# Kernel tuning notes

Measured on AMD Instinct MI355X. Metric: run time of the kernel, lower is better.

## Reference

```python
import jax, jax.numpy as jnp
import numpy as np

A, NA, D_OBS, B = 16, 8, 64, 128  # agents, actions, obs dim, graphs
DZ = D_OBS + NA  # obs_z_input_dim = 72


def _mlp(x, W1, b1, W2, b2):
    # Linear -> leaky_relu(0.01) -> Linear, torch Linear convention (y = x @ W.T + b)
    return jax.nn.leaky_relu(x @ W1.T + b1) @ W2.T + b2


def setup_inputs() -> dict:
    key = jax.random.key(0)
    ks = iter(jax.random.split(key, 40))
    p = {}
    p["obs"] = jax.random.normal(next(ks), (B * A, D_OBS), jnp.float32)
    p["policies"] = jax.random.uniform(next(ks), (B * A, NA), jnp.float32)
    p["actions"] = jax.random.uniform(next(ks), (B * A, NA), jnp.float32)

    def mk(name, inp, out):
        p[name + "_w"] = jax.random.normal(next(ks), (out, inp), jnp.float32) / np.sqrt(inp).astype(np.float32)
        p[name + "_b"] = jax.random.normal(next(ks), (out,), jnp.float32) * 0.01

    mk("kw1", D_OBS, 64); mk("kw2", 64, 64)   # key_weight layers
    mk("qw1", D_OBS, 64); mk("qw2", 64, 64)   # query_weight layers
    mk("ko1", DZ, 64);    mk("ko2", 64, 64)   # key_obsz layers
    mk("qo1", DZ, 64);    mk("qo2", 64, 64)   # query_obsz layers
    mk("av1", DZ, 64);    mk("av2", 64, 64)   # attention_value_obsz layers
    mk("fv1", 128, 64);   mk("fv2", 64, 8)    # final_value layers
    return p


def reference(obs, policies, actions,
              kw1_w, kw1_b, kw2_w, kw2_b, qw1_w, qw1_b, qw2_w, qw2_b,
              ko1_w, ko1_b, ko2_w, ko2_b, qo1_w, qo1_b, qo2_w, qo2_b,
              av1_w, av1_b, av2_w, av2_b, fv1_w, fv1_b, fv2_w, fv2_b):
    d_k_w = jnp.sqrt(jnp.float32(kw2_w.shape[0]))
    d_k_o = jnp.sqrt(jnp.float32(ko2_w.shape[0]))
    Bn = obs.shape[0] // A
    obs_b = obs.reshape(Bn, A, -1)                      # [B,A,Dobs]
    pi = policies.reshape(Bn, A, NA)
    act = actions.reshape(Bn, A, NA)

    # --- DGL update_all on the fully-connected (with self-loop) per-batch graph ---
    key_z = _mlp(obs_b, kw1_w, kw1_b, kw2_w, kw2_b)     # [B,A,dk]
    query_z = _mlp(obs_b, qw1_w, qw1_b, qw2_w, qw2_b)
    score = jnp.einsum('bjd,bid->bij', key_z, query_z)  # src key j -> dst query i
    w = jax.nn.sigmoid(score / d_k_w)[..., None]        # [B,A,A,1], mailbox gate
    z = w * act[:, None] + (1.0 - w) * pi[:, None]      # [B,A(i),A(j),NA]
    weight_z = w.reshape(Bn * A, A, 1)

    # obs_z[b,i,j] = cat(obs[b,j], z[b,i,j])
    obs_rep = jnp.broadcast_to(obs_b[:, None], (Bn, A, A, obs_b.shape[-1]))
    obs_z = jnp.concatenate([obs_rep, z], axis=-1)      # [B,A,A,DZ]

    diag = jnp.arange(A)
    src = obs_z[:, diag, diag]                          # source_obs_z_: [B,A,DZ] (j==i entry)

    key_o = _mlp(src, ko1_w, ko1_b, ko2_w, ko2_b)       # broadcast over j
    query_o = _mlp(obs_z, qo1_w, qo1_b, qo2_w, qo2_b)   # [B,A,A,dk]
    score_o = jnp.einsum('bid,bijd->bij', key_o, query_o)
    weights_o = jax.nn.softmax(jnp.exp(jnp.clip(score_o / d_k_o, -5.0, 5.0)), axis=-1)  # [B,A,A]

    # obs_z_pi[b,i,j,k] = op[b,j] if k==j else obs_z[b,i,k], op = cat(obs, pi)
    op = jnp.concatenate([obs_b, pi], axis=-1)          # [B,A,DZ]
    m = jnp.eye(A, dtype=obs.dtype)[None, None, :, :, None]          # (j,k) mask
    obs_z_pi = obs_z[:, :, None] * (1.0 - m) + op[:, None, None] * m  # [B,A,A,A,DZ]

    attn_src = _mlp(src, av1_w, av1_b, av2_w, av2_b)                  # [B,A,O]
    attn_other = _mlp(obs_z_pi, av1_w, av1_b, av2_w, av2_b)           # [B,A,A,A,O]

    w_exp = weights_o[:, None, :, :, None]              # [b,i,j,k,1] = weights_o[b,j,k]
    mixed = jnp.mean(attn_other * w_exp, axis=-2)       # mean over k -> [B,A,A,O]
    src_rep = jnp.broadcast_to(attn_src[:, None], mixed.shape)
    node_features = jnp.concatenate([src_rep, mixed], axis=-1)        # [B,A,A,2O]
    value = _mlp(node_features, fv1_w, fv1_b, fv2_w, fv2_b)           # [B,A,A,8]

    weights_obsz = jnp.broadcast_to(w_exp, (Bn, A, A, A, 1))
    return value, weight_z, weights_obsz
```

## Files before the change

kernel.cpp:

```cpp
#include <hip/hip_runtime.h>

#define A_ 16
#define NA_ 8
#define DOBS_ 64

typedef _Float16 f16;
typedef f16 h2 __attribute__((ext_vector_type(2)));
typedef f16 v8h __attribute__((ext_vector_type(8)));
typedef float v4f __attribute__((ext_vector_type(4)));

__device__ __forceinline__ float fdot2f(h2 a, h2 b, float c) {
  return __builtin_amdgcn_fdot2(a, b, c, false);
}
__device__ __forceinline__ float lrelu(float x) { return x > 0.f ? x : 0.01f * x; }

struct P {
  const float *obs, *pol, *act;
  const float *kw1w, *kw1b, *kw2w, *kw2b, *qw1w, *qw1b, *qw2w, *qw2b;
  const float *ko1w, *ko1b, *ko2w, *ko2b, *qo1w, *qo1b, *qo2w, *qo2b;
  const float *av1w, *av1b, *av2w, *av2b, *fv1w, *fv1b, *fv2w, *fv2b;
  float *out0, *out1, *out2;
};

#define OBSH 0
#define OBSL 1152
#define X1Ho 2304
#define X1Lo 3456
#define X2Ho 4608
#define X2Lo 5760
#define EHO  6912
#define FLT  7168
#define F_PI   0
#define F_ACT  128
#define F_WSIG 256
#define F_WO   512
#define F_C0   768
#define F_S2   784
#define F_S3G  1872
#define F_WZK  2960
#define F_WZQ  3472
#define WKW1  15136
#define WQW1  19744
#define WKW2  24352
#define WQW2  28960
#define WKO1H 33568
#define WKO1L 38176
#define WKO2H 42784
#define WKO2L 47392
#define WQO1H 52000
#define WQO1L 56608
#define WQO2H 61216
#define WQO2L 65824
#define LDS_F16 70432
#define AV1H  15136
#define AV2H  21280
#define FV1H  25888
#define FV2PW 34592
#define BACKB 35104
#define SLICE 52000
#define AOSRC 64288
#define APTO  65440
#define AEXT  66976

__device__ __forceinline__ v4f gemm_plain(const f16* Xh, const f16* W, float bv, int nt, int lane) {
  const int m = lane & 15, q = lane >> 4;
  v4f acc = {bv, bv, bv, bv};
  const v8h a0 = *(const v8h*)(Xh + m * 72 + q * 8);
  const v8h a1 = *(const v8h*)(Xh + m * 72 + 32 + q * 8);
  const f16* wr = W + (nt * 16 + m) * 72 + q * 8;
  acc = __builtin_amdgcn_mfma_f32_16x16x32_f16(a0, *(const v8h*)wr, acc, 0, 0, 0);
  acc = __builtin_amdgcn_mfma_f32_16x16x32_f16(a1, *(const v8h*)(wr + 32), acc, 0, 0, 0);
  return acc;
}

__device__ __forceinline__ v4f gemm_tile(const f16* Xh, const f16* Xl,
                                         const f16* Wh, const f16* Wl,
                                         float bv, int nt, int lane) {
  const int m = lane & 15, q = lane >> 4;
  v4f acc = {bv, bv, bv, bv};
  const v8h ah0 = *(const v8h*)(Xh + m * 72 + q * 8);
  const v8h ah1 = *(const v8h*)(Xh + m * 72 + 32 + q * 8);
  const v8h al0 = *(const v8h*)(Xl + m * 72 + q * 8);
  const v8h al1 = *(const v8h*)(Xl + m * 72 + 32 + q * 8);
  const f16* wr = Wh + (nt * 16 + m) * 72 + q * 8;
  const v8h bh0 = *(const v8h*)(wr);
  const v8h bh1 = *(const v8h*)(wr + 32);
  const f16* wr2 = Wl + (nt * 16 + m) * 72 + q * 8;
  const v8h bl0 = *(const v8h*)(wr2);
  const v8h bl1 = *(const v8h*)(wr2 + 32);
  acc = __builtin_amdgcn_mfma_f32_16x16x32_f16(ah0, bh0, acc, 0, 0, 0);
  acc = __builtin_amdgcn_mfma_f32_16x16x32_f16(ah1, bh1, acc, 0, 0, 0);
  acc = __builtin_amdgcn_mfma_f32_16x16x32_f16(ah0, bl0, acc, 0, 0, 0);
  acc = __builtin_amdgcn_mfma_f32_16x16x32_f16(ah1, bl1, acc, 0, 0, 0);
  acc = __builtin_amdgcn_mfma_f32_16x16x32_f16(al0, bh0, acc, 0, 0, 0);
  acc = __builtin_amdgcn_mfma_f32_16x16x32_f16(al1, bh1, acc, 0, 0, 0);
  return acc;
}

__device__ __forceinline__ void writeX(f16* Xh, f16* Xl, v4f acc, int nt, int lane, bool relu) {
  const int m = lane & 15, q = lane >> 4;
#pragma unroll
  for (int reg = 0; reg < 4; reg++) {
    float y = acc[reg];
    if (relu) y = lrelu(y);
    const f16 yh = (f16)y;
    Xh[(q * 4 + reg) * 72 + nt * 16 + m] = yh;
    Xl[(q * 4 + reg) * 72 + nt * 16 + m] = (f16)(y - (float)yh);
  }
}

__device__ __forceinline__ void putP(f16* W, float4 v, int o, int rq) {
  h2* d = (h2*)(W + o * 72 + 4 * rq);
  d[0] = h2{(f16)v.x, (f16)v.y};
  d[1] = h2{(f16)v.z, (f16)v.w};
}

__device__ __forceinline__ void putW(f16* Wh, f16* Wl, float4 v, int o, int rq) {
  h2* dh = (h2*)(Wh + o * 72 + 4 * rq);
  h2* dl = (h2*)(Wl + o * 72 + 4 * rq);
  const f16 hx = (f16)v.x, hy = (f16)v.y, hz = (f16)v.z, hw = (f16)v.w;
  dh[0] = h2{hx, hy};
  dh[1] = h2{hz, hw};
  dl[0] = h2{(f16)(v.x - (float)hx), (f16)(v.y - (float)hy)};
  dl[1] = h2{(f16)(v.z - (float)hz), (f16)(v.w - (float)hw)};
}

__device__ __forceinline__ v8h bfrag(const f16* Wm, int stride, int nt, int ks, int lane) {
  const int n = lane & 15, q = lane >> 4;
  return *(const v8h*)(Wm + (nt * 16 + n) * stride + ks * 32 + q * 8);
}

__device__ __forceinline__ void av_mlp2(const f16* obsh, const f16* av1H, const f16* av2H,
                                        const float* av1b, const float* av2b,
                                        f16* Hbuf, v8h az, int lane, v4f acc2[4]) {
  const int m = lane & 15, q = lane >> 4;
  const v8h a0 = *(const v8h*)(obsh + m * 72 + q * 8);
  const v8h a1 = *(const v8h*)(obsh + m * 72 + 32 + q * 8);
#pragma unroll
  for (int nt = 0; nt < 4; nt++) {
    const float bv = av1b[nt * 16 + m];
    v4f acc = {bv, bv, bv, bv};
    acc = __builtin_amdgcn_mfma_f32_16x16x32_f16(a0, bfrag(av1H, 96, nt, 0, lane), acc, 0, 0, 0);
    acc = __builtin_amdgcn_mfma_f32_16x16x32_f16(a1, bfrag(av1H, 96, nt, 1, lane), acc, 0, 0, 0);
    acc = __builtin_amdgcn_mfma_f32_16x16x32_f16(az, bfrag(av1H, 96, nt, 2, lane), acc, 0, 0, 0);
#pragma unroll
    for (int reg = 0; reg < 4; reg++)
      Hbuf[(q * 4 + reg) * 72 + nt * 16 + m] = (f16)lrelu(acc[reg]);
  }
  const v8h h0 = *(const v8h*)(Hbuf + m * 72 + q * 8);
  const v8h h1 = *(const v8h*)(Hbuf + m * 72 + 32 + q * 8);
#pragma unroll
  for (int nt = 0; nt < 4; nt++) {
    const float bv = av2b[nt * 16 + m];
    v4f acc = {bv, bv, bv, bv};
    acc = __builtin_amdgcn_mfma_f32_16x16x32_f16(h0, bfrag(av2H, 72, nt, 0, lane), acc, 0, 0, 0);
    acc = __builtin_amdgcn_mfma_f32_16x16x32_f16(h1, bfrag(av2H, 72, nt, 1, lane), acc, 0, 0, 0);
    acc2[nt] = acc;
  }
}

__global__ __launch_bounds__(512) void critic_fused(P p) {
  extern __shared__ f16 SMB[];
  float* F = (float*)(SMB + FLT);
  const int tid = threadIdx.x;
  const int b = blockIdx.x >> 1, ihalf = blockIdx.x & 1;
  const int w = tid >> 6, lane = tid & 63;
  const int m = lane & 15, quad = lane >> 4;
  const int o = tid & 63, r8 = tid >> 6;

  const float2 Robs = ((const float2*)(p.obs + (size_t)b * 1024))[tid];
  float Rpa = 0.f;
  if (tid < 128) Rpa = p.pol[(size_t)b * 128 + tid];
  else if (tid < 256) Rpa = p.act[(size_t)b * 128 + tid - 128];
  const float Rwzko = p.ko1w[(tid >> 3) * 72 + 64 + (tid & 7)];
  const float Rwzqo = p.qo1w[(tid >> 3) * 72 + 64 + (tid & 7)];
  float4 Rkw1[2], Rqw1[2], Rkw2[2], Rqw2[2], Rko1[2], Rko2[2], Rqo1[2], Rqo2[2];
#pragma unroll
  for (int h = 0; h < 2; h++) {
    const int rq = r8 + 8 * h;
    Rkw1[h] = *(const float4*)(p.kw1w + o * 64 + 4 * rq);
    Rqw1[h] = *(const float4*)(p.qw1w + o * 64 + 4 * rq);
    Rkw2[h] = *(const float4*)(p.kw2w + o * 64 + 4 * rq);
    Rqw2[h] = *(const float4*)(p.qw2w + o * 64 + 4 * rq);
    Rko1[h] = *(const float4*)(p.ko1w + o * 72 + 4 * rq);
    Rko2[h] = *(const float4*)(p.ko2w + o * 64 + 4 * rq);
    Rqo1[h] = *(const float4*)(p.qo1w + o * 72 + 4 * rq);
    Rqo2[h].x = p.qo2w[(4 * rq + 0) * 64 + o];
    Rqo2[h].y = p.qo2w[(4 * rq + 1) * 64 + o];
    Rqo2[h].z = p.qo2w[(4 * rq + 2) * 64 + o];
    Rqo2[h].w = p.qo2w[(4 * rq + 3) * 64 + o];
  }
  const int bi = (w & 3) * 16 + m;
  const float bias1 = (w < 4 ? p.kw1b : p.qw1b)[bi];
  const float bias2 = (w < 4 ? p.kw2b : p.qw2b)[bi];
  const float bias3 = (w < 4 ? p.ko1b : p.qo1b)[bi];
  const float bias4 = p.ko2b[bi];
  const float Bqo2_0 = p.qo2b[tid & 31];
  const float Bqo2_1 = p.qo2b[(tid & 31) + 32];

  {
    const int e0 = 2 * tid, r0 = e0 >> 6, c0i = e0 & 63;
    const f16 hx = (f16)Robs.x, hy = (f16)Robs.y;
    *(h2*)(SMB + OBSH + r0 * 72 + c0i) = h2{hx, hy};
    *(h2*)(SMB + OBSL + r0 * 72 + c0i) = h2{(f16)(Robs.x - (float)hx), (f16)(Robs.y - (float)hy)};
  }
  if (tid < 128) F[F_PI + tid] = Rpa;
  else if (tid < 256) F[F_ACT + tid - 128] = Rpa;
  F[F_WZK + tid] = Rwzko;
  { const int oo = tid >> 3, c = tid & 7; F[F_WZQ + (oo & 15) * 32 + (oo >> 4) * 8 + c] = Rwzqo; }
#pragma unroll
  for (int h = 0; h < 2; h++) {
    const int rq = r8 + 8 * h;
    putP(SMB + WKW1, Rkw1[h], o, rq);
    putP(SMB + WQW1, Rqw1[h], o, rq);
    putP(SMB + WKW2, Rkw2[h], o, rq);
    putP(SMB + WQW2, Rqw2[h], o, rq);
    putW(SMB + WKO1H, SMB + WKO1L, Rko1[h], o, rq);
    putW(SMB + WKO2H, SMB + WKO2L, Rko2[h], o, rq);
    putW(SMB + WQO1H, SMB + WQO1L, Rqo1[h], o, rq);
    putW(SMB + WQO2H, SMB + WQO2L, Rqo2[h], o, rq);
  }
  __syncthreads();

  {
    const f16* Wp = (w < 4) ? (SMB + WKW1) : (SMB + WQW1);
    f16* Xo = (w < 4) ? (SMB + X1Ho) : (SMB + X2Ho);
    v4f a = gemm_plain(SMB + OBSH, Wp, bias1, w & 3, lane);
#pragma unroll
    for (int reg = 0; reg < 4; reg++)
      Xo[(quad * 4 + reg) * 72 + (w & 3) * 16 + m] = (f16)lrelu(a[reg]);
  }
  __syncthreads();

  {
    const f16* Wp = (w < 4) ? (SMB + WKW2) : (SMB + WQW2);
    const f16* Xi = (w < 4) ? (SMB + X1Ho) : (SMB + X2Ho);
    float* So = (w < 4) ? (F + F_S2) : (F + F_S3G);
    v4f a = gemm_plain(Xi, Wp, bias2, w & 3, lane);
#pragma unroll
    for (int reg = 0; reg < 4; reg++)
      So[(quad * 4 + reg) * 68 + (w & 3) * 16 + m] = a[reg];
  }
  __syncthreads();

  {
    const int idx = tid >> 1, g2 = tid & 1;
    const int i = idx >> 4, j = idx & 15;
    float a0 = 0.f, a1 = 0.f, a2 = 0.f, a3 = 0.f;
#pragma unroll
    for (int t4 = 0; t4 < 8; t4++) {
      const float4 qv = *(const float4*)(F + F_S3G + i * 68 + g2 * 32 + 4 * t4);
      const float4 kv = *(const float4*)(F + F_S2 + j * 68 + g2 * 32 + 4 * t4);
      a0 += qv.x * kv.x; a1 += qv.y * kv.y; a2 += qv.z * kv.z; a3 += qv.w * kv.w;
    }
    float sc = (a0 + a1) + (a2 + a3);
    sc += __shfl_xor(sc, 1);
    if (g2 == 0) {
      const float wv = 1.f / (1.f + __expf(-sc * 0.125f));
      F[F_WSIG + idx] = wv;
      p.out1[(size_t)b * 256 + idx] = wv;
    }
  }
  __syncthreads();

  if (w < 4) {
    v4f a = gemm_tile(SMB + OBSH, SMB + OBSL, SMB + WKO1H, SMB + WKO1L, bias3, w, lane);
    const int oo = w * 16 + m;
    float wzv[8];
    *(float4*)wzv = *(const float4*)(F + F_WZK + oo * 8);
    *(float4*)(wzv + 4) = *(const float4*)(F + F_WZK + oo * 8 + 4);
#pragma unroll
    for (int reg = 0; reg < 4; reg++) {
      const int rr = quad * 4 + reg;
      const float wrr = F[F_WSIG + rr * 16 + rr];
      float zp = 0.f;
#pragma unroll
      for (int c = 0; c < 8; c++) {
        const float zc = F[F_PI + rr * 8 + c] + wrr * (F[F_ACT + rr * 8 + c] - F[F_PI + rr * 8 + c]);
        zp += wzv[c] * zc;
      }
      const float y = lrelu(a[reg] + zp);
      const f16 yh = (f16)y;
      SMB[X2Ho + rr * 72 + oo] = yh;
      SMB[X2Lo + rr * 72 + oo] = (f16)(y - (float)yh);
    }
  } else {
    v4f a = gemm_tile(SMB + OBSH, SMB + OBSL, SMB + WQO1H, SMB + WQO1L, bias3, w - 4, lane);
#pragma unroll
    for (int reg = 0; reg < 4; reg++)
      F[F_S3G + m * 68 + (quad * 4 + reg) * 4 + (w - 4)] = a[reg];
  }
  __syncthreads();

  const float4 rav1a = ((const float4*)p.av1w)[tid * 2];
  const float4 rav1b = ((const float4*)p.av1w)[tid * 2 + 1];
  const float rav1c = p.av1w[4096 + tid];
  const float4 rav2a = ((const float4*)p.av2w)[tid * 2];
  const float4 rav2b = ((const float4*)p.av2w)[tid * 2 + 1];
  const float rfv2 = p.fv2w[tid];
  float rb1 = 0.f, rb2 = 0.f, rb3 = 0.f, rb4 = 0.f;
  if (tid < 64) { rb1 = p.av1b[tid]; rb2 = p.av2b[tid]; rb3 = p.fv1b[tid]; }
  if (tid < 8) rb4 = p.fv2b[tid];
  if (w < 4) {
    v4f a = gemm_tile(SMB + X2Ho, SMB + X2Lo, SMB + WKO2H, SMB + WKO2L, bias4, w, lane);
    writeX(SMB + X1Ho, SMB + X1Lo, a, w, lane, false);
  }
  __syncthreads();

  float4 rfv[4];
#pragma unroll
  for (int qq = 0; qq < 4; qq++) rfv[qq] = ((const float4*)p.fv1w)[tid * 4 + qq];
  if (w < 4) {
    v4f a = gemm_tile(SMB + X1Ho, SMB + X1Lo, SMB + WQO2H, SMB + WQO2L, 0.f, w, lane);
#pragma unroll
    for (int reg = 0; reg < 4; reg++)
      F[F_S2 + (quad * 4 + reg) * 68 + w * 16 + m] = a[reg];
  }
  {
    const int rr = tid >> 5, cc = tid & 31;
    const float kv0 = (float)SMB[X1Ho + rr * 72 + cc] + (float)SMB[X1Lo + rr * 72 + cc];
    const float kv1 = (float)SMB[X1Ho + rr * 72 + cc + 32] + (float)SMB[X1Lo + rr * 72 + cc + 32];
    float t = kv0 * Bqo2_0 + kv1 * Bqo2_1;
#pragma unroll
    for (int mk = 1; mk < 32; mk <<= 1) t += __shfl_xor(t, mk);
    if (cc == 0) F[F_C0 + rr] = t;
  }
  __syncthreads();

  {
    const int idx = tid >> 1, g2 = tid & 1;
    const int i = idx >> 4, j = idx & 15;
    const float wij = F[F_WSIG + i * 16 + j];
    float z[8];
#pragma unroll
    for (int c = 0; c < 8; c++)
      z[c] = F[F_PI + j * 8 + c] + wij * (F[F_ACT + j * 8 + c] - F[F_PI + j * 8 + c]);
    float sc = 0.f;
#pragma unroll
    for (int gg = 2 * g2; gg <= 2 * g2 + 1; gg++) {
#pragma unroll
      for (int t = 0; t < 16; t++) {
        const float4 wa = *(const float4*)(F + F_WZQ + t * 32 + gg * 8);
        const float4 wb = *(const float4*)(F + F_WZQ + t * 32 + gg * 8 + 4);
        float hv = F[F_S3G + t * 68 + j * 4 + gg]
          + wa.x * z[0] + wa.y * z[1] + wa.z * z[2] + wa.w * z[3]
          + wb.x * z[4] + wb.y * z[5] + wb.z * z[6] + wb.w * z[7];
        hv = lrelu(hv);
        sc += F[F_S2 + i * 68 + gg * 16 + t] * hv;
      }
    }
    sc += __shfl_xor(sc, 1);
    if (g2 == 0) {
      float yv = (sc + F[F_C0 + i]) * 0.125f;
      yv = fminf(fmaxf(yv, -5.f), 5.f);
      SMB[EHO + idx] = (f16)__expf(yv);
    }
  }
  __syncthreads();

  if (tid < 256) {
    const int i = tid >> 4, j = tid & 15;
    float ev[16]; float mx = -1e30f;
#pragma unroll
    for (int jj = 0; jj < 16; jj++) { ev[jj] = (float)SMB[EHO + i * 16 + jj]; mx = fmaxf(mx, ev[jj]); }
    float den = 0.f;
#pragma unroll
    for (int jj = 0; jj < 16; jj++) den += __expf(ev[jj] - mx);
    F[F_WO + tid] = __expf(ev[j] - mx) / den;
  }
  {
    float av1v[8] = {rav1a.x, rav1a.y, rav1a.z, rav1a.w, rav1b.x, rav1b.y, rav1b.z, rav1b.w};
#pragma unroll
    for (int e = 0; e < 8; e++) {
      const int k = tid * 8 + e, rr = k / 72, cc = k - rr * 72;
      SMB[AV1H + rr * 96 + cc] = (f16)av1v[e];
    }
    const int k = 4096 + tid, rr = k / 72, cc = k - rr * 72;
    SMB[AV1H + rr * 96 + cc] = (f16)rav1c;
    const int row = tid >> 3, c0p = 72 + (tid & 7) * 3;
#pragma unroll
    for (int c = 0; c < 3; c++) SMB[AV1H + row * 96 + c0p + c] = (f16)0.f;
    float av2v[8] = {rav2a.x, rav2a.y, rav2a.z, rav2a.w, rav2b.x, rav2b.y, rav2b.z, rav2b.w};
#pragma unroll
    for (int e = 0; e < 8; e++) {
      const int k2 = tid * 8 + e;
      SMB[AV2H + (k2 >> 6) * 72 + (k2 & 63)] = (f16)av2v[e];
    }
    SMB[FV2PW + tid] = (f16)rfv2;
    float* BF = (float*)(SMB + BACKB);
    if (tid < 64) { BF[tid] = rb1; BF[64 + tid] = rb2; BF[128 + tid] = rb3; }
    if (tid < 8) BF[192 + tid] = rb4;
  }
  __syncthreads();

  {
    const int kk = tid >> 5, j2 = tid & 31;
    float v = 0.f;
    if (j2 < 16) v = F[F_WO + kk * 16 + j2] * 0.0625f;
    else if (j2 - 16 == kk) v = F[F_WO + kk * 16 + kk] * 0.0625f;
    SMB[AEXT + kk * 40 + j2] = (f16)v;
    const int q_ = tid >> 1, g2_ = tid & 1, k_ = q_ & 15;
    float* dst = p.out2 + ((size_t)b * 256 + q_) * 16 + 8 * g2_;
    *(float4*)(dst) = *(const float4*)(F + F_WO + k_ * 16 + 8 * g2_);
    *(float4*)(dst + 4) = *(const float4*)(F + F_WO + k_ * 16 + 8 * g2_ + 4);
  }
  __syncthreads();

#pragma unroll
  for (int qq = 0; qq < 4; qq++) {
    const int e0 = tid * 16 + qq * 4;
    h2* d = (h2*)&SMB[FV1H + (e0 >> 7) * 136 + (e0 & 127)];
    d[0] = h2{(f16)rfv[qq].x, (f16)rfv[qq].y};
    d[1] = h2{(f16)rfv[qq].z, (f16)rfv[qq].w};
  }
  const float* BF = (const float*)(SMB + BACKB);
  const int i_ = ihalf * 8 + w;
  f16* Sl = SMB + SLICE + w * 1536;
  {
    v8h az = {};
    if (quad == 0) {
      const float wv = F[F_WSIG + i_ * 16 + m];
#pragma unroll
      for (int c = 0; c < 8; c++)
        az[c] = (f16)(F[F_PI + m * 8 + c] + wv * (F[F_ACT + m * 8 + c] - F[F_PI + m * 8 + c]));
    }
    v4f acc2[4];
    av_mlp2(SMB + OBSH, SMB + AV1H, SMB + AV2H, BF, BF + 64, Sl, az, lane, acc2);
#pragma unroll
    for (int nt = 0; nt < 4; nt++)
#pragma unroll
      for (int reg = 0; reg < 4; reg++)
        Sl[(nt * 16 + m) * 24 + quad * 4 + reg] = (f16)acc2[nt][reg];
  }
  if (w == 0) {
    v8h az = {};
    if (quad == 0) {
#pragma unroll
      for (int c = 0; c < 8; c++) az[c] = (f16)F[F_PI + m * 8 + c];
    }
    v4f acc2[4];
    av_mlp2(SMB + OBSH, SMB + AV1H, SMB + AV2H, BF, BF + 64, SMB + APTO, az, lane, acc2);
#pragma unroll
    for (int nt = 0; nt < 4; nt++)
#pragma unroll
      for (int reg = 0; reg < 4; reg++)
        SMB[APTO + (nt * 16 + m) * 24 + quad * 4 + reg] = (f16)acc2[nt][reg];
  }
  if (w == 1) {
    v8h az = {};
    if (quad == 0) {
      const float wv = F[F_WSIG + m * 16 + m];
#pragma unroll
      for (int c = 0; c < 8; c++)
        az[c] = (f16)(F[F_PI + m * 8 + c] + wv * (F[F_ACT + m * 8 + c] - F[F_PI + m * 8 + c]));
    }
    v4f acc2[4];
    av_mlp2(SMB + OBSH, SMB + AV1H, SMB + AV2H, BF, BF + 64, SMB + AOSRC, az, lane, acc2);
#pragma unroll
    for (int nt = 0; nt < 4; nt++)
#pragma unroll
      for (int reg = 0; reg < 4; reg++)
        SMB[AOSRC + (quad * 4 + reg) * 72 + nt * 16 + m] = (f16)acc2[nt][reg];
  }
  __syncthreads();

  {
    const v8h am = *(const v8h*)(&SMB[AEXT + m * 40 + quad * 8]);
    v4f macc[4];
#pragma unroll
    for (int nt = 0; nt < 4; nt++) {
      const int oo = nt * 16 + m;
      v8h bf;
      if (quad < 2) {
        bf = *(const v8h*)(Sl + oo * 24 + quad * 8);
      } else {
        const v8h apv = *(const v8h*)(&SMB[APTO + oo * 24 + (quad - 2) * 8]);
        const v8h aov = *(const v8h*)(Sl + oo * 24 + (quad - 2) * 8);
        bf = apv - aov;
      }
      v4f z4 = {0.f, 0.f, 0.f, 0.f};
      macc[nt] = __builtin_amdgcn_mfma_f32_16x16x32_f16(am, bf, z4, 0, 0, 0);
    }
#pragma unroll
    for (int nt = 0; nt < 4; nt++)
#pragma unroll
      for (int reg = 0; reg < 4; reg++)
        Sl[(quad * 4 + reg) * 72 + nt * 16 + m] = (f16)macc[nt][reg];
  }
  {
    const v8h f0 = *(const v8h*)(&SMB[AOSRC + m * 72 + quad * 8]);
    const v8h f1 = *(const v8h*)(&SMB[AOSRC + m * 72 + 32 + quad * 8]);
    const v8h f2 = *(const v8h*)(Sl + m * 72 + quad * 8);
    const v8h f3 = *(const v8h*)(Sl + m * 72 + 32 + quad * 8);
#pragma unroll
    for (int nt = 0; nt < 4; nt++) {
      const float bv = BF[128 + nt * 16 + m];
      v4f acc = {bv, bv, bv, bv};
      acc = __builtin_amdgcn_mfma_f32_16x16x32_f16(f0, bfrag(SMB + FV1H, 136, nt, 0, lane), acc, 0, 0, 0);
      acc = __builtin_amdgcn_mfma_f32_16x16x32_f16(f1, bfrag(SMB + FV1H, 136, nt, 1, lane), acc, 0, 0, 0);
      acc = __builtin_amdgcn_mfma_f32_16x16x32_f16(f2, bfrag(SMB + FV1H, 136, nt, 2, lane), acc, 0, 0, 0);
      acc = __builtin_amdgcn_mfma_f32_16x16x32_f16(f3, bfrag(SMB + FV1H, 136, nt, 3, lane), acc, 0, 0, 0);
#pragma unroll
      for (int reg = 0; reg < 4; reg++)
        Sl[(quad * 4 + reg) * 72 + nt * 16 + m] = (f16)lrelu(acc[reg]);
    }
  }
  {
    const int g2 = quad;
    float y0 = BF[192 + 2 * g2], y1 = BF[192 + 2 * g2 + 1];
#pragma unroll
    for (int o2 = 0; o2 < 32; o2++) {
      const h2 hh = *(const h2*)(Sl + m * 72 + 2 * o2);
      const h2 w0 = *(const h2*)(&SMB[FV2PW + (2 * g2) * 64 + 2 * o2]);
      const h2 w1 = *(const h2*)(&SMB[FV2PW + (2 * g2 + 1) * 64 + 2 * o2]);
      y0 = fdot2f(w0, hh, y0);
      y1 = fdot2f(w1, hh, y1);
    }
    *(float2*)(p.out0 + ((size_t)b * 256 + i_ * 16 + m) * 8 + 2 * g2) = make_float2(y0, y1);
  }
}

extern "C" void kernel_launch(void* const* d_in, const int* in_sizes, int n_in,
                              void* d_out, int out_size, void* d_ws, size_t ws_size,
                              hipStream_t stream) {
  P p;
  p.obs = (const float*)d_in[0];
  p.pol = (const float*)d_in[1];
  p.act = (const float*)d_in[2];
  p.kw1w = (const float*)d_in[3];  p.kw1b = (const float*)d_in[4];
  p.kw2w = (const float*)d_in[5];  p.kw2b = (const float*)d_in[6];
  p.qw1w = (const float*)d_in[7];  p.qw1b = (const float*)d_in[8];
  p.qw2w = (const float*)d_in[9];  p.qw2b = (const float*)d_in[10];
  p.ko1w = (const float*)d_in[11]; p.ko1b = (const float*)d_in[12];
  p.ko2w = (const float*)d_in[13]; p.ko2b = (const float*)d_in[14];
  p.qo1w = (const float*)d_in[15]; p.qo1b = (const float*)d_in[16];
  p.qo2w = (const float*)d_in[17]; p.qo2b = (const float*)d_in[18];
  p.av1w = (const float*)d_in[19]; p.av1b = (const float*)d_in[20];
  p.av2w = (const float*)d_in[21]; p.av2b = (const float*)d_in[22];
  p.fv1w = (const float*)d_in[23]; p.fv1b = (const float*)d_in[24];
  p.fv2w = (const float*)d_in[25]; p.fv2b = (const float*)d_in[26];

  const int Bn = in_sizes[0] / (A_ * DOBS_);
  p.out0 = (float*)d_out;
  p.out1 = p.out0 + (size_t)Bn * A_ * A_ * NA_;
  p.out2 = p.out1 + (size_t)Bn * A_ * A_;

  const size_t lds_bytes = (size_t)LDS_F16 * sizeof(f16);
  (void)hipFuncSetAttribute(reinterpret_cast<const void*>(critic_fused),
                            hipFuncAttributeMaxDynamicSharedMemorySize, (int)lds_bytes);
  hipLaunchKernelGGL(critic_fused, dim3(2 * Bn), dim3(512), lds_bytes, stream, p);
}
```

Before: 125.3 us.

## Overlap attention-value MLP with key/query chain via warp specialization

Reorganizes the post-sigmoid phase so warp 0 runs the whole ko1→ko2→qo2 chain, warp 1 runs qo1, and the remaining six warps run the attention-value MLP tasks concurrently, instead of spreading each stage over eight warps with barriers in between. All weight and bias loads are hoisted to the start of the kernel, and the av weights are staged into LDS earlier, with a new LDS layout holding separate slice buffers. Several __syncthreads are removed and the out2 store is folded into the final per-warp stage. The serial dependency chain on warp 0 and the larger LDS footprint (reducing occupancy) may offset the gain from overlap.

```diff
diff --git a/kernel.cpp b/kernel.cpp
--- a/kernel.cpp
+++ b/kernel.cpp
@@ -39,28 +39,30 @@
 #define F_S3G  1872
 #define F_WZK  2960
 #define F_WZQ  3472
-#define WKW1  15136
-#define WQW1  19744
-#define WKW2  24352
-#define WQW2  28960
-#define WKO1H 33568
-#define WKO1L 38176
-#define WKO2H 42784
-#define WKO2L 47392
-#define WQO1H 52000
-#define WQO1L 56608
-#define WQO2H 61216
-#define WQO2L 65824
-#define LDS_F16 70432
-#define AV1H  15136
-#define AV2H  21280
-#define FV1H  25888
-#define FV2PW 34592
-#define BACKB 35104
-#define SLICE 52000
-#define AOSRC 64288
-#define APTO  65440
-#define AEXT  66976
+#define F_B    3984
+#define WKW1  15648
+#define WQW1  20256
+#define WKW2  24864
+#define WQW2  29472
+#define WKO1H 34080
+#define WKO1L 38688
+#define WKO2H 43296
+#define WKO2L 47904
+#define WQO1H 52512
+#define WQO1L 57120
+#define WQO2H 61728
+#define WQO2L 66336
+#define AV1H  15648
+#define AV2H  21792
+#define BACKB1 26400
+#define SLA   26656
+#define SLB   70944
+#define AOSRC 77088
+#define APTO  78240
+#define FV1H  34080
+#define FV2PW 42784
+#define BACKB2 43296
+#define LDS_F16 79776
 
 __device__ __forceinline__ v4f gemm_plain(const f16* Xh, const f16* W, float bv, int nt, int lane) {
   const int m = lane & 15, q = lane >> 4;
@@ -193,10 +195,20 @@
   const int bi = (w & 3) * 16 + m;
   const float bias1 = (w < 4 ? p.kw1b : p.qw1b)[bi];
   const float bias2 = (w < 4 ? p.kw2b : p.qw2b)[bi];
-  const float bias3 = (w < 4 ? p.ko1b : p.qo1b)[bi];
-  const float bias4 = p.ko2b[bi];
-  const float Bqo2_0 = p.qo2b[tid & 31];
-  const float Bqo2_1 = p.qo2b[(tid & 31) + 32];
+  float rbo1 = 0.f, rbo2 = 0.f, rbo3 = 0.f, rbo4 = 0.f;
+  if (tid < 64) { rbo1 = p.ko1b[tid]; rbo2 = p.ko2b[tid]; rbo3 = p.qo1b[tid]; rbo4 = p.qo2b[tid]; }
+  const float4 rav1a = ((const float4*)p.av1w)[tid * 2];
+  const float4 rav1b = ((const float4*)p.av1w)[tid * 2 + 1];
+  const float rav1c = p.av1w[4096 + tid];
+  const float4 rav2a = ((const float4*)p.av2w)[tid * 2];
+  const float4 rav2b = ((const float4*)p.av2w)[tid * 2 + 1];
+  float4 rfv[4];
+#pragma unroll
+  for (int qq = 0; qq < 4; qq++) rfv[qq] = ((const float4*)p.fv1w)[tid * 4 + qq];
+  const float rfv2 = p.fv2w[tid];
+  float rb1 = 0.f, rb2 = 0.f, rb3 = 0.f, rb4 = 0.f;
+  if (tid < 64) { rb1 = p.av1b[tid]; rb2 = p.av2b[tid]; rb3 = p.fv1b[tid]; }
+  if (tid < 8) rb4 = p.fv2b[tid];
 
   {
     const int e0 = 2 * tid, r0 = e0 >> 6, c0i = e0 & 63;
@@ -208,6 +220,10 @@
   else if (tid < 256) F[F_ACT + tid - 128] = Rpa;
   F[F_WZK + tid] = Rwzko;
   { const int oo = tid >> 3, c = tid & 7; F[F_WZQ + (oo & 15) * 32 + (oo >> 4) * 8 + c] = Rwzqo; }
+  if (tid < 64) {
+    F[F_B + tid] = rbo1; F[F_B + 64 + tid] = rbo2;
+    F[F_B + 128 + tid] = rbo3; F[F_B + 192 + tid] = rbo4;
+  }
 #pragma unroll
   for (int h = 0; h < 2; h++) {
     const int rq = r8 + 8 * h;
@@ -261,69 +277,131 @@
       p.out1[(size_t)b * 256 + idx] = wv;
     }
   }
-  __syncthreads();
-
-  if (w < 4) {
-    v4f a = gemm_tile(SMB + OBSH, SMB + OBSL, SMB + WKO1H, SMB + WKO1L, bias3, w, lane);
-    const int oo = w * 16 + m;
-    float wzv[8];
-    *(float4*)wzv = *(const float4*)(F + F_WZK + oo * 8);
-    *(float4*)(wzv + 4) = *(const float4*)(F + F_WZK + oo * 8 + 4);
-#pragma unroll
-    for (int reg = 0; reg < 4; reg++) {
-      const int rr = quad * 4 + reg;
-      const float wrr = F[F_WSIG + rr * 16 + rr];
-      float zp = 0.f;
-#pragma unroll
-      for (int c = 0; c < 8; c++) {
-        const float zc = F[F_PI + rr * 8 + c] + wrr * (F[F_ACT + rr * 8 + c] - F[F_PI + rr * 8 + c]);
-        zp += wzv[c] * zc;
-      }
-      const float y = lrelu(a[reg] + zp);
-      const f16 yh = (f16)y;
-      SMB[X2Ho + rr * 72 + oo] = yh;
-      SMB[X2Lo + rr * 72 + oo] = (f16)(y - (float)yh);
+  {
+    float av1v[8] = {rav1a.x, rav1a.y, rav1a.z, rav1a.w, rav1b.x, rav1b.y, rav1b.z, rav1b.w};
+#pragma unroll
+    for (int e = 0; e < 8; e++) {
+      const int k = tid * 8 + e, rr = k / 72, cc = k - rr * 72;
+      SMB[AV1H + rr * 96 + cc] = (f16)av1v[e];
+    }
+    const int k = 4096 + tid, rr = k / 72, cc = k - rr * 72;
+    SMB[AV1H + rr * 96 + cc] = (f16)rav1c;
+    const int row = tid >> 3, c0p = 72 + (tid & 7) * 3;
+#pragma unroll
+    for (int c = 0; c < 3; c++) SMB[AV1H + row * 96 + c0p + c] = (f16)0.f;
+    float av2v[8] = {rav2a.x, rav2a.y, rav2a.z, rav2a.w, rav2b.x, rav2b.y, rav2b.z, rav2b.w};
+#pragma unroll
+    for (int e = 0; e < 8; e++) {
+      const int k2 = tid * 8 + e;
+      SMB[AV2H + (k2 >> 6) * 72 + (k2 & 63)] = (f16)av2v[e];
+    }
+    float* BF1 = (float*)(SMB + BACKB1);
+    if (tid < 64) { BF1[tid] = rb1; BF1[64 + tid] = rb2; }
+  }
+  __syncthreads();
+
+  const float* BF1 = (const float*)(SMB + BACKB1);
+  if (w == 0) {
+#pragma unroll
+    for (int nt = 0; nt < 4; nt++) {
+      v4f a = gemm_tile(SMB + OBSH, SMB + OBSL, SMB + WKO1H, SMB + WKO1L, F[F_B + nt * 16 + m], nt, lane);
+      const int oo = nt * 16 + m;
+      float wzv[8];
+      *(float4*)wzv = *(const float4*)(F + F_WZK + oo * 8);
+      *(float4*)(wzv + 4) = *(const float4*)(F + F_WZK + oo * 8 + 4);
+#pragma unroll
+      for (int reg = 0; reg < 4; reg++) {
+        const int rr = quad * 4 + reg;
+        const float wrr = F[F_WSIG + rr * 17];
+        float zp = 0.f;
+#pragma unroll
+        for (int c = 0; c < 8; c++) {
+          const float zc = F[F_PI + rr * 8 + c] + wrr * (F[F_ACT + rr * 8 + c] - F[F_PI + rr * 8 + c]);
+          zp += wzv[c] * zc;
+        }
+        const float y = lrelu(a[reg] + zp);
+        const f16 yh = (f16)y;
+        SMB[X2Ho + rr * 72 + oo] = yh;
+        SMB[X2Lo + rr * 72 + oo] = (f16)(y - (float)yh);
+      }
+    }
+#pragma unroll
+    for (int nt = 0; nt < 4; nt++) {
+      v4f a = gemm_tile(SMB + X2Ho, SMB + X2Lo, SMB + WKO2H, SMB + WKO2L, F[F_B + 64 + nt * 16 + m], nt, lane);
+      writeX(SMB + X1Ho, SMB + X1Lo, a, nt, lane, false);
+    }
+#pragma unroll
+    for (int nt = 0; nt < 4; nt++) {
+      v4f a = gemm_tile(SMB + X1Ho, SMB + X1Lo, SMB + WQO2H, SMB + WQO2L, 0.f, nt, lane);
+#pragma unroll
+      for (int reg = 0; reg < 4; reg++)
+        F[F_S2 + (quad * 4 + reg) * 68 + nt * 16 + m] = a[reg];
+    }
+    {
+      const int r = lane >> 2, cs = (lane & 3) * 16;
+      float t = 0.f;
+#pragma unroll
+      for (int c = 0; c < 16; c++) {
+        const float kv = (float)SMB[X1Ho + r * 72 + cs + c] + (float)SMB[X1Lo + r * 72 + cs + c];
+        t += kv * F[F_B + 192 + cs + c];
+      }
+      t += __shfl_xor(t, 1);
+      t += __shfl_xor(t, 2);
+      if ((lane & 3) == 0) F[F_C0 + r] = t;
+    }
+  } else if (w == 1) {
+#pragma unroll
+    for (int nt = 0; nt < 4; nt++) {
+      v4f a = gemm_tile(SMB + OBSH, SMB + OBSL, SMB + WQO1H, SMB + WQO1L, F[F_B + 128 + nt * 16 + m], nt, lane);
+#pragma unroll
+      for (int reg = 0; reg < 4; reg++)
+        F[F_S3G + m * 68 + (quad * 4 + reg) * 4 + nt] = a[reg];
     }
   } else {
-    v4f a = gemm_tile(SMB + OBSH, SMB + OBSL, SMB + WQO1H, SMB + WQO1L, bias3, w - 4, lane);
-#pragma unroll
-    for (int reg = 0; reg < 4; reg++)
-      F[F_S3G + m * 68 + (quad * 4 + reg) * 4 + (w - 4)] = a[reg];
-  }
-  __syncthreads();
-
-  const float4 rav1a = ((const float4*)p.av1w)[tid * 2];
-  const float4 rav1b = ((const float4*)p.av1w)[tid * 2 + 1];
-  const float rav1c = p.av1w[4096 + tid];
-  const float4 rav2a = ((const float4*)p.av2w)[tid * 2];
-  const float4 rav2b = ((const float4*)p.av2w)[tid * 2 + 1];
-  const float rfv2 = p.fv2w[tid];
-  float rb1 = 0.f, rb2 = 0.f, rb3 = 0.f, rb4 = 0.f;
-  if (tid < 64) { rb1 = p.av1b[tid]; rb2 = p.av2b[tid]; rb3 = p.fv1b[tid]; }
-  if (tid < 8) rb4 = p.fv2b[tid];
-  if (w < 4) {
-    v4f a = gemm_tile(SMB + X2Ho, SMB + X2Lo, SMB + WKO2H, SMB + WKO2L, bias4, w, lane);
-    writeX(SMB + X1Ho, SMB + X1Lo, a, w, lane, false);
-  }
-  __syncthreads();
-
-  float4 rfv[4];
-#pragma unroll
-  for (int qq = 0; qq < 4; qq++) rfv[qq] = ((const float4*)p.fv1w)[tid * 4 + qq];
-  if (w < 4) {
-    v4f a = gemm_tile(SMB + X1Ho, SMB + X1Lo, SMB + WQO2H, SMB + WQO2L, 0.f, w, lane);
-#pragma unroll
-    for (int reg = 0; reg < 4; reg++)
-      F[F_S2 + (quad * 4 + reg) * 68 + w * 16 + m] = a[reg];
-  }
-  {
-    const int rr = tid >> 5, cc = tid & 31;
-    const float kv0 = (float)SMB[X1Ho + rr * 72 + cc] + (float)SMB[X1Lo + rr * 72 + cc];
-    const float kv1 = (float)SMB[X1Ho + rr * 72 + cc + 32] + (float)SMB[X1Lo + rr * 72 + cc + 32];
-    float t = kv0 * Bqo2_0 + kv1 * Bqo2_1;
-#pragma unroll
-    for (int mk = 1; mk < 32; mk <<= 1) t += __shfl_xor(t, mk);
-    if (cc == 0) F[F_C0 + rr] = t;
+    auto do_task = [&](int t) {
+      f16* Hb;
+      v8h az = {};
+      if (t < 8) {
+        Hb = (t < 4) ? (SMB + SLA + t * 1536) : (SMB + SLB + (t - 4) * 1536);
+        if (quad == 0) {
+          const float wv = F[F_WSIG + (ihalf * 8 + t) * 16 + m];
+#pragma unroll
+          for (int c = 0; c < 8; c++)
+            az[c] = (f16)(F[F_PI + m * 8 + c] + wv * (F[F_ACT + m * 8 + c] - F[F_PI + m * 8 + c]));
+        }
+      } else if (t == 8) {
+        Hb = SMB + APTO;
+        if (quad == 0) {
+#pragma unroll
+          for (int c = 0; c < 8; c++) az[c] = (f16)F[F_PI + m * 8 + c];
+        }
+      } else {
+        Hb = SMB + AOSRC;
+        if (quad == 0) {
+          const float wv = F[F_WSIG + m * 17];
+#pragma unroll
+          for (int c = 0; c < 8; c++)
+            az[c] = (f16)(F[F_PI + m * 8 + c] + wv * (F[F_ACT + m * 8 + c] - F[F_PI + m * 8 + c]));
+        }
+      }
+      v4f acc2[4];
+      av_mlp2(SMB + OBSH, SMB + AV1H, SMB + AV2H, BF1, BF1 + 64, Hb, az, lane, acc2);
+      if (t < 9) {
+#pragma unroll
+        for (int nt = 0; nt < 4; nt++)
+#pragma unroll
+          for (int reg = 0; reg < 4; reg++)
+            Hb[(nt * 16 + m) * 24 + quad * 4 + reg] = (f16)acc2[nt][reg];
+      } else {
+#pragma unroll
+        for (int nt = 0; nt < 4; nt++)
+#pragma unroll
+          for (int reg = 0; reg < 4; reg++)
+            SMB[AOSRC + (quad * 4 + reg) * 72 + nt * 16 + m] = (f16)acc2[nt][reg];
+      }
+    };
+    do_task(w - 2);
+    if (w - 2 < 4) do_task(w - 2 + 6);
   }
   __syncthreads();
 
@@ -356,56 +434,6 @@
       SMB[EHO + idx] = (f16)__expf(yv);
     }
   }
-  __syncthreads();
-
-  if (tid < 256) {
-    const int i = tid >> 4, j = tid & 15;
-    float ev[16]; float mx = -1e30f;
-#pragma unroll
-    for (int jj = 0; jj < 16; jj++) { ev[jj] = (float)SMB[EHO + i * 16 + jj]; mx = fmaxf(mx, ev[jj]); }
-    float den = 0.f;
-#pragma unroll
-    for (int jj = 0; jj < 16; jj++) den += __expf(ev[jj] - mx);
-    F[F_WO + tid] = __expf(ev[j] - mx) / den;
-  }
-  {
-    float av1v[8] = {rav1a.x, rav1a.y, rav1a.z, rav1a.w, rav1b.x, rav1b.y, rav1b.z, rav1b.w};
-#pragma unroll
-    for (int e = 0; e < 8; e++) {
-      const int k = tid * 8 + e, rr = k / 72, cc = k - rr * 72;
-      SMB[AV1H + rr * 96 + cc] = (f16)av1v[e];
-    }
-    const int k = 4096 + tid, rr = k / 72, cc = k - rr * 72;
-    SMB[AV1H + rr * 96 + cc] = (f16)rav1c;
-    const int row = tid >> 3, c0p = 72 + (tid & 7) * 3;
-#pragma unroll
-    for (int c = 0; c < 3; c++) SMB[AV1H + row * 96 + c0p + c] = (f16)0.f;
-    float av2v[8] = {rav2a.x, rav2a.y, rav2a.z, rav2a.w, rav2b.x, rav2b.y, rav2b.z, rav2b.w};
-#pragma unroll
-    for (int e = 0; e < 8; e++) {
-      const int k2 = tid * 8 + e;
-      SMB[AV2H + (k2 >> 6) * 72 + (k2 & 63)] = (f16)av2v[e];
-    }
-    SMB[FV2PW + tid] = (f16)rfv2;
-    float* BF = (float*)(SMB + BACKB);
-    if (tid < 64) { BF[tid] = rb1; BF[64 + tid] = rb2; BF[128 + tid] = rb3; }
-    if (tid < 8) BF[192 + tid] = rb4;
-  }
-  __syncthreads();
-
-  {
-    const int kk = tid >> 5, j2 = tid & 31;
-    float v = 0.f;
-    if (j2 < 16) v = F[F_WO + kk * 16 + j2] * 0.0625f;
-    else if (j2 - 16 == kk) v = F[F_WO + kk * 16 + kk] * 0.0625f;
-    SMB[AEXT + kk * 40 + j2] = (f16)v;
-    const int q_ = tid >> 1, g2_ = tid & 1, k_ = q_ & 15;
-    float* dst = p.out2 + ((size_t)b * 256 + q_) * 16 + 8 * g2_;
-    *(float4*)(dst) = *(const float4*)(F + F_WO + k_ * 16 + 8 * g2_);
-    *(float4*)(dst + 4) = *(const float4*)(F + F_WO + k_ * 16 + 8 * g2_ + 4);
-  }
-  __syncthreads();
-
 #pragma unroll
   for (int qq = 0; qq < 4; qq++) {
     const int e0 = tid * 16 + qq * 4;
@@ -413,110 +441,96 @@
     d[0] = h2{(f16)rfv[qq].x, (f16)rfv[qq].y};
     d[1] = h2{(f16)rfv[qq].z, (f16)rfv[qq].w};
   }
-  const float* BF = (const float*)(SMB + BACKB);
-  const int i_ = ihalf * 8 + w;
-  f16* Sl = SMB + SLICE + w * 1536;
-  {
-    v8h az = {};
-    if (quad == 0) {
-      const float wv = F[F_WSIG + i_ * 16 + m];
-#pragma unroll
-      for (int c = 0; c < 8; c++)
-        az[c] = (f16)(F[F_PI + m * 8 + c] + wv * (F[F_ACT + m * 8 + c] - F[F_PI + m * 8 + c]));
-    }
-    v4f acc2[4];
-    av_mlp2(SMB + OBSH, SMB + AV1H, SMB + AV2H, BF, BF + 64, Sl, az, lane, acc2);
-#pragma unroll
-    for (int nt = 0; nt < 4; nt++)
-#pragma unroll
-      for (int reg = 0; reg < 4; reg++)
-        Sl[(nt * 16 + m) * 24 + quad * 4 + reg] = (f16)acc2[nt][reg];
-  }
-  if (w == 0) {
-    v8h az = {};
-    if (quad == 0) {
-#pragma unroll
-      for (int c = 0; c < 8; c++) az[c] = (f16)F[F_PI + m * 8 + c];
-    }
-    v4f acc2[4];
-    av_mlp2(SMB + OBSH, SMB + AV1H, SMB + AV2H, BF, BF + 64, SMB + APTO, az, lane, acc2);
-#pragma unroll
-    for (int nt = 0; nt < 4; nt++)
-#pragma unroll
-      for (int reg = 0; reg < 4; reg++)
-        SMB[APTO + (nt * 16 + m) * 24 + quad * 4 + reg] = (f16)acc2[nt][reg];
-  }
-  if (w == 1) {
-    v8h az = {};
-    if (quad == 0) {
-      const float wv = F[F_WSIG + m * 16 + m];
-#pragma unroll
-      for (int c = 0; c < 8; c++)
-        az[c] = (f16)(F[F_PI + m * 8 + c] + wv * (F[F_ACT + m * 8 + c] - F[F_PI + m * 8 + c]));
-    }
-    v4f acc2[4];
-    av_mlp2(SMB + OBSH, SMB + AV1H, SMB + AV2H, BF, BF + 64, SMB + AOSRC, az, lane, acc2);
-#pragma unroll
-    for (int nt = 0; nt < 4; nt++)
-#pragma unroll
-      for (int reg = 0; reg < 4; reg++)
-        SMB[AOSRC + (quad * 4 + reg) * 72 + nt * 16 + m] = (f16)acc2[nt][reg];
-  }
-  __syncthreads();
-
-  {
-    const v8h am = *(const v8h*)(&SMB[AEXT + m * 40 + quad * 8]);
-    v4f macc[4];
-#pragma unroll
-    for (int nt = 0; nt < 4; nt++) {
-      const int oo = nt * 16 + m;
-      v8h bf;
-      if (quad < 2) {
-        bf = *(const v8h*)(Sl + oo * 24 + quad * 8);
-      } else {
-        const v8h apv = *(const v8h*)(&SMB[APTO + oo * 24 + (quad - 2) * 8]);
-        const v8h aov = *(const v8h*)(Sl + oo * 24 + (quad - 2) * 8);
-        bf = apv - aov;
-      }
-      v4f z4 = {0.f, 0.f, 0.f, 0.f};
-      macc[nt] = __builtin_amdgcn_mfma_f32_16x16x32_f16(am, bf, z4, 0, 0, 0);
-    }
-#pragma unroll
-    for (int nt = 0; nt < 4; nt++)
-#pragma unroll
-      for (int reg = 0; reg < 4; reg++)
-        Sl[(quad * 4 + reg) * 72 + nt * 16 + m] = (f16)macc[nt][reg];
-  }
-  {
-    const v8h f0 = *(const v8h*)(&SMB[AOSRC + m * 72 + quad * 8]);
-    const v8h f1 = *(const v8h*)(&SMB[AOSRC + m * 72 + 32 + quad * 8]);
-    const v8h f2 = *(const v8h*)(Sl + m * 72 + quad * 8);
-    const v8h f3 = *(const v8h*)(Sl + m * 72 + 32 + quad * 8);
-#pragma unroll
-    for (int nt = 0; nt < 4; nt++) {
-      const float bv = BF[128 + nt * 16 + m];
-      v4f acc = {bv, bv, bv, bv};
-      acc = __builtin_amdgcn_mfma_f32_16x16x32_f16(f0, bfrag(SMB + FV1H, 136, nt, 0, lane), acc, 0, 0, 0);
-      acc = __builtin_amdgcn_mfma_f32_16x16x32_f16(f1, bfrag(SMB + FV1H, 136, nt, 1, lane), acc, 0, 0, 0);
-      acc = __builtin_amdgcn_mfma_f32_16x16x32_f16(f2, bfrag(SMB + FV1H, 136, nt, 2, lane), acc, 0, 0, 0);
-      acc = __builtin_amdgcn_mfma_f32_16x16x32_f16(f3, bfrag(SMB + FV1H, 136, nt, 3, lane), acc, 0, 0, 0);
-#pragma unroll
-      for (int reg = 0; reg < 4; reg++)
-        Sl[(quad * 4 + reg) * 72 + nt * 16 + m] = (f16)lrelu(acc[reg]);
-    }
-  }
-  {
-    const int g2 = quad;
-    float y0 = BF[192 + 2 * g2], y1 = BF[192 + 2 * g2 + 1];
-#pragma unroll
-    for (int o2 = 0; o2 < 32; o2++) {
-      const h2 hh = *(const h2*)(Sl + m * 72 + 2 * o2);
-      const h2 w0 = *(const h2*)(&SMB[FV2PW + (2 * g2) * 64 + 2 * o2]);
-      const h2 w1 = *(const h2*)(&SMB[FV2PW + (2 * g2 + 1) * 64 + 2 * o2]);
-      y0 = fdot2f(w0, hh, y0);
-      y1 = fdot2f(w1, hh, y1);
-    }
-    *(float2*)(p.out0 + ((size_t)b * 256 + i_ * 16 + m) * 8 + 2 * g2) = make_float2(y0, y1);
+  SMB[FV2PW + tid] = (f16)rfv2;
+  {
+    float* BF2 = (float*)(SMB + BACKB2);
+    if (tid < 64) BF2[tid] = rb3;
+    if (tid < 8) BF2[64 + tid] = rb4;
+  }
+  __syncthreads();
+
+  if (tid < 256) {
+    const int i = tid >> 4, j = tid & 15;
+    float ev[16]; float mx = -1e30f;
+#pragma unroll
+    for (int jj = 0; jj < 16; jj++) { ev[jj] = (float)SMB[EHO + i * 16 + jj]; mx = fmaxf(mx, ev[jj]); }
+    float den = 0.f;
+#pragma unroll
+    for (int jj = 0; jj < 16; jj++) den += __expf(ev[jj] - mx);
+    F[F_WO + tid] = __expf(ev[j] - mx) / den;
+  }
+  __syncthreads();
+
+  {
+    const float* BF2 = (const float*)(SMB + BACKB2);
+    const int i_ = ihalf * 8 + w;
+    f16* Sl = (w < 4) ? (SMB + SLA + w * 1536) : (SMB + SLB + (w - 4) * 1536);
+    v8h am;
+#pragma unroll
+    for (int e = 0; e < 8; e++) {
+      const int j2 = quad * 8 + e;
+      float v;
+      if (j2 < 16) v = F[F_WO + m * 16 + j2] * 0.0625f;
+      else v = (j2 - 16 == m) ? F[F_WO + m * 17] * 0.0625f : 0.f;
+      am[e] = (f16)v;
+    }
+    {
+      v4f macc[4];
+#pragma unroll
+      for (int nt = 0; nt < 4; nt++) {
+        const int oo = nt * 16 + m;
+        v8h bf;
+        if (quad < 2) {
+          bf = *(const v8h*)(Sl + oo * 24 + quad * 8);
+        } else {
+          const v8h apv = *(const v8h*)(&SMB[APTO + oo * 24 + (quad - 2) * 8]);
+          const v8h aov = *(const v8h*)(Sl + oo * 24 + (quad - 2) * 8);
+          bf = apv - aov;
+        }
+        v4f z4 = {0.f, 0.f, 0.f, 0.f};
+        macc[nt] = __builtin_amdgcn_mfma_f32_16x16x32_f16(am, bf, z4, 0, 0, 0);
+      }
+#pragma unroll
+      for (int nt = 0; nt < 4; nt++)
+#pragma unroll
+        for (int reg = 0; reg < 4; reg++)
+          Sl[(quad * 4 + reg) * 72 + nt * 16 + m] = (f16)macc[nt][reg];
+    }
+    {
+      const v8h f0 = *(const v8h*)(&SMB[AOSRC + m * 72 + quad * 8]);
+      const v8h f1 = *(const v8h*)(&SMB[AOSRC + m * 72 + 32 + quad * 8]);
+      const v8h f2 = *(const v8h*)(Sl + m * 72 + quad * 8);
+      const v8h f3 = *(const v8h*)(Sl + m * 72 + 32 + quad * 8);
+#pragma unroll
+      for (int nt = 0; nt < 4; nt++) {
+        const float bv = BF2[nt * 16 + m];
+        v4f acc = {bv, bv, bv, bv};
+        acc = __builtin_amdgcn_mfma_f32_16x16x32_f16(f0, bfrag(SMB + FV1H, 136, nt, 0, lane), acc, 0, 0, 0);
+        acc = __builtin_amdgcn_mfma_f32_16x16x32_f16(f1, bfrag(SMB + FV1H, 136, nt, 1, lane), acc, 0, 0, 0);
+        acc = __builtin_amdgcn_mfma_f32_16x16x32_f16(f2, bfrag(SMB + FV1H, 136, nt, 2, lane), acc, 0, 0, 0);
+        acc = __builtin_amdgcn_mfma_f32_16x16x32_f16(f3, bfrag(SMB + FV1H, 136, nt, 3, lane), acc, 0, 0, 0);
+#pragma unroll
+        for (int reg = 0; reg < 4; reg++)
+          Sl[(quad * 4 + reg) * 72 + nt * 16 + m] = (f16)lrelu(acc[reg]);
+      }
+    }
+    {
+      const int g2 = quad;
+      float y0 = BF2[64 + 2 * g2], y1 = BF2[64 + 2 * g2 + 1];
+#pragma unroll
+      for (int o2 = 0; o2 < 32; o2++) {
+        const h2 hh = *(const h2*)(Sl + m * 72 + 2 * o2);
+        const h2 w0v = *(const h2*)(&SMB[FV2PW + (2 * g2) * 64 + 2 * o2]);
+        const h2 w1v = *(const h2*)(&SMB[FV2PW + (2 * g2 + 1) * 64 + 2 * o2]);
+        y0 = fdot2f(w0v, hh, y0);
+        y1 = fdot2f(w1v, hh, y1);
+      }
+      *(float2*)(p.out0 + ((size_t)b * 256 + i_ * 16 + m) * 8 + 2 * g2) = make_float2(y0, y1);
+    }
+    {
+      const float4 wv4 = *(const float4*)(F + F_WO + m * 16 + quad * 4);
+      *(float4*)(p.out2 + ((size_t)b * 256 + i_ * 16 + m) * 16 + quad * 4) = wv4;
+    }
   }
 }
 
```

After: 131.0 us. +4.5%, slower.
